# Optimization experiments

Measured on AMD Instinct MI355X. Metric: run time of the kernel, lower is better.

## Reference

```python
import jax, jax.numpy as jnp
import numpy as np

N_HEAD = 16
N_FEAT = 1024
D_K = N_FEAT // N_HEAD
BATCH = 8
SEQ = 1024
LN_EPS = 1e-5
MIN_VAL = float(np.finfo(np.float32).min)


def setup_inputs() -> dict:
    key = jax.random.key(0)
    ks = jax.random.split(key, 8)
    s = 0.02  # small init scale for weights to keep activations sane
    return {
        "x": jax.random.normal(ks[0], (BATCH, SEQ, N_FEAT), jnp.float32),
        "pos_k": jax.random.normal(ks[1], (SEQ, SEQ, D_K), jnp.float32) * s,
        "mask": jnp.ones((BATCH, SEQ, SEQ), jnp.int32),
        "ln_scale": jnp.ones((N_FEAT,), jnp.float32),
        "ln_bias": jnp.zeros((N_FEAT,), jnp.float32),
        "wq": jax.random.normal(ks[2], (N_FEAT, N_FEAT), jnp.float32) * s,
        "bq": jnp.zeros((N_FEAT,), jnp.float32),
        "wk": jax.random.normal(ks[3], (N_FEAT, N_FEAT), jnp.float32) * s,
        "bk": jnp.zeros((N_FEAT,), jnp.float32),
        "wv": jax.random.normal(ks[4], (N_FEAT, N_FEAT), jnp.float32) * s,
        "bv": jnp.zeros((N_FEAT,), jnp.float32),
        "wo": jax.random.normal(ks[5], (N_FEAT, N_FEAT), jnp.float32) * s,
        "bo": jnp.zeros((N_FEAT,), jnp.float32),
    }


def reference(x, pos_k, mask, ln_scale, ln_bias, wq, bq, wk, bk, wv, bv, wo, bo):
    b, t, f = x.shape
    h, d = N_HEAD, D_K
    # LayerNorm over feature dim
    mu = jnp.mean(x, axis=-1, keepdims=True)
    var = jnp.mean((x - mu) ** 2, axis=-1, keepdims=True)
    xn = (x - mu) / jnp.sqrt(var + LN_EPS) * ln_scale + ln_bias
    # QKV projections (torch Linear: y = x @ W^T + b), split heads -> (b, h, t, d)
    q = (xn @ wq.T + bq).reshape(b, t, h, d).transpose(0, 2, 1, 3)
    k = (xn @ wk.T + bk).reshape(b, t, h, d).transpose(0, 2, 1, 3)
    v = (xn @ wv.T + bv).reshape(b, t, h, d).transpose(0, 2, 1, 3)
    # content score A and relative-position score B
    A = jnp.einsum("bhtd,bhsd->bhts", q, k)
    B = jnp.einsum("bhtd,tsd->bhts", q, pos_k)
    scores = (A + B) / jnp.sqrt(jnp.asarray(d, scores_dtype := x.dtype))
    m = (mask[:, None, :, :] == 0)  # (b, 1, t, s) broadcast over heads
    scores = jnp.where(m, MIN_VAL, scores)
    attn = jax.nn.softmax(scores, axis=-1)
    attn = jnp.where(m, 0.0, attn)
    out = jnp.einsum("bhts,bhsd->bhtd", attn, v)
    out = out.transpose(0, 2, 1, 3).reshape(b, t, h * d)
    return out @ wo.T + bo
```

## Files before the change

kernel.cpp:

```cpp
#include <hip/hip_runtime.h>
#include <hip/hip_bf16.h>

typedef unsigned short ushort_t;
typedef short short8 __attribute__((ext_vector_type(8)));
typedef unsigned short ushort8 __attribute__((ext_vector_type(8)));
typedef unsigned short ushortx4 __attribute__((ext_vector_type(4)));
typedef float fx4 __attribute__((ext_vector_type(4)));
typedef int ix4 __attribute__((ext_vector_type(4)));

#define MFMA(a, b, c) __builtin_amdgcn_mfma_f32_16x16x32_bf16((a), (b), (c), 0, 0, 0)

#define QSCALE 0.18033688011112042f

__device__ __forceinline__ ushort_t f2bf(float f) {
  __hip_bfloat16 h = __float2bfloat16(f);
  return *(ushort_t*)&h;
}
__device__ __forceinline__ float bf2f(ushort_t h) {
  union { unsigned u; float f; } c; c.u = ((unsigned)h) << 16;
  return c.f;
}
__device__ __forceinline__ void gload16(const ushort_t* g, ushort_t* l) {
  __builtin_amdgcn_global_load_lds((const __attribute__((address_space(1))) void*)g,
                                   (__attribute__((address_space(3))) void*)l, 16, 0, 0);
}

__global__ __launch_bounds__(256) void cvt4_kernel(const float* __restrict__ s0,
                                                   const float* __restrict__ s1,
                                                   const float* __restrict__ s2,
                                                   const float* __restrict__ s3,
                                                   ushort_t* __restrict__ d0,
                                                   ushort_t* __restrict__ d1,
                                                   ushort_t* __restrict__ d2,
                                                   ushort_t* __restrict__ d3) {
  int bi = blockIdx.x;
  const float* src = (bi < 1024) ? s0 : (bi < 2048) ? s1 : (bi < 3072) ? s2 : s3;
  ushort_t* dst = (bi < 1024) ? d0 : (bi < 2048) ? d1 : (bi < 3072) ? d2 : d3;
  int i = (bi & 1023) * 256 + threadIdx.x;
  fx4 v = *(const fx4*)&src[(size_t)i * 4];
  ushortx4 o;
#pragma unroll
  for (int j = 0; j < 4; ++j) o[j] = f2bf(v[j]);
  *(ushortx4*)&dst[(size_t)i * 4] = o;
}

__global__ __launch_bounds__(256) void ln_kernel(const float* __restrict__ x,
                                                 const float* __restrict__ sc,
                                                 const float* __restrict__ bi,
                                                 ushort_t* __restrict__ xn) {
  __shared__ float red[8];
  int row = blockIdx.x, tid = threadIdx.x;
  const float* xr = x + (size_t)row * 1024;
  fx4 v = *(const fx4*)&xr[tid * 4];
  float s = v[0] + v[1] + v[2] + v[3];
  float s2 = v[0] * v[0] + v[1] * v[1] + v[2] * v[2] + v[3] * v[3];
#pragma unroll
  for (int m = 32; m >= 1; m >>= 1) {
    s += __shfl_xor(s, m);
    s2 += __shfl_xor(s2, m);
  }
  int wave = tid >> 6;
  if ((tid & 63) == 0) { red[wave * 2] = s; red[wave * 2 + 1] = s2; }
  __syncthreads();
  s = red[0] + red[2] + red[4] + red[6];
  s2 = red[1] + red[3] + red[5] + red[7];
  float mu = s * (1.f / 1024.f);
  float var = s2 * (1.f / 1024.f) - mu * mu;
  float rs = rsqrtf(var + 1e-5f);
  fx4 scv = *(const fx4*)&sc[tid * 4];
  fx4 biv = *(const fx4*)&bi[tid * 4];
  ushortx4 o;
#pragma unroll
  for (int j = 0; j < 4; ++j) o[j] = f2bf((v[j] - mu) * rs * scv[j] + biv[j]);
  *(ushortx4*)&xn[(size_t)row * 1024 + tid * 4] = o;
}

__global__ __launch_bounds__(256) void maskpack_kernel(const int* __restrict__ mask,
                                                       unsigned* __restrict__ bits) {
  __shared__ unsigned char nib[256];
  int row = blockIdx.x, tid = threadIdx.x;
  ix4 m = *(const ix4*)&mask[(size_t)row * 1024 + tid * 4];
  nib[tid] = (unsigned char)((m[0] != 0 ? 1 : 0) | (m[1] != 0 ? 2 : 0) |
                             (m[2] != 0 ? 4 : 0) | (m[3] != 0 ? 8 : 0));
  __syncthreads();
  if (tid < 32) {
    unsigned w = 0;
#pragma unroll
    for (int j = 0; j < 8; ++j) w |= ((unsigned)nib[tid * 8 + j]) << (j * 4);
    bits[(size_t)row * 32 + tid] = w;
  }
}

template <int F32OUT>
__global__ __launch_bounds__(256) void gemm_bt(const ushort_t* __restrict__ A,
                                               const ushort_t* __restrict__ B,
                                               const float* __restrict__ bias, void* C,
                                               int M, int N, int K, float oscale) {
  __shared__ ushort_t lA[4096];
  __shared__ ushort_t lB[4096];
  int bm = blockIdx.y * 128, bn = blockIdx.x * 128;
  int tid = threadIdx.x;
  int wave = tid >> 6, lane = tid & 63;
  int wm = (wave >> 1) * 64, wn = (wave & 1) * 64;
  int l15 = lane & 15, lg = lane >> 4;
  int r0 = tid >> 2, c0 = (tid & 3) * 8;
  int g1 = 256 + tid, r1 = g1 >> 2, c1 = (g1 & 3) * 8;
  int lb0 = (wave * 64) * 8;
  int lb1 = (256 + wave * 64) * 8;
  fx4 acc[4][4] = {};
  for (int k0 = 0; k0 < K; k0 += 32) {
    __syncthreads();
    gload16(&A[(size_t)(bm + r0) * K + k0 + c0], &lA[lb0]);
    gload16(&A[(size_t)(bm + r1) * K + k0 + c1], &lA[lb1]);
    gload16(&B[(size_t)(bn + r0) * K + k0 + c0], &lB[lb0]);
    gload16(&B[(size_t)(bn + r1) * K + k0 + c1], &lB[lb1]);
    __syncthreads();
    short8 af[4], bf[4];
#pragma unroll
    for (int i = 0; i < 4; ++i) af[i] = *(const short8*)&lA[(wm + i * 16 + l15) * 32 + lg * 8];
#pragma unroll
    for (int i = 0; i < 4; ++i) bf[i] = *(const short8*)&lB[(wn + i * 16 + l15) * 32 + lg * 8];
#pragma unroll
    for (int i = 0; i < 4; ++i)
#pragma unroll
      for (int j = 0; j < 4; ++j) acc[i][j] = MFMA(af[i], bf[j], acc[i][j]);
  }
#pragma unroll
  for (int j = 0; j < 4; ++j) {
    int n = bn + wn + j * 16 + l15;
    float bv = bias[n];
#pragma unroll
    for (int i = 0; i < 4; ++i) {
      int mr = bm + wm + i * 16 + lg * 4;
#pragma unroll
      for (int r = 0; r < 4; ++r) {
        float val = (acc[i][j][r] + bv) * oscale;
        if (F32OUT)
          ((float*)C)[(size_t)(mr + r) * N + n] = val;
        else
          ((ushort_t*)C)[(size_t)(mr + r) * N + n] = f2bf(val);
      }
    }
  }
}

__device__ __forceinline__ void loadset(const float* base, int c, fx4* r) {
  const float* p = base + (size_t)c * 1024;
  r[0] = *(const fx4*)p;
  r[1] = *(const fx4*)(p + 4);
  r[2] = *(const fx4*)(p + 32);
  r[3] = *(const fx4*)(p + 36);
}
__device__ __forceinline__ void cvtset(const fx4* r, short8& f0, short8& f1) {
#pragma unroll
  for (int j = 0; j < 4; ++j) {
    f0[j] = (short)f2bf(r[0][j]); f0[j + 4] = (short)f2bf(r[1][j]);
    f1[j] = (short)f2bf(r[2][j]); f1[j + 4] = (short)f2bf(r[3][j]);
  }
}

__global__ __launch_bounds__(256, 3) void ball_kernel(const ushort_t* __restrict__ q,
                                                      const float* __restrict__ pos_k,
                                                      ushort_t* __restrict__ B_all) {
  __shared__ ushort_t lq[128 * 64];
  int t = blockIdx.y, sx = blockIdx.x;
  int tid = threadIdx.x, wave = tid >> 6, lane = tid & 63, l15 = lane & 15, lg = lane >> 4;
  const float* pk = pos_k + (size_t)t * 65536;
  int sw = sx * 512 + wave * 128;
  const float* base = pk + (size_t)(sw + l15) * 64 + lg * 8;

  fx4 raw[4][4];
#pragma unroll
  for (int c = 0; c < 4; ++c) loadset(base, c, raw[c]);

#pragma unroll
  for (int it = 0; it < 4; ++it) {
    int u = tid + it * 256;
    int row = u >> 3, cu = u & 7;
    ushort8 vv = *(const ushort8*)&q[((size_t)((row >> 4) * 1024 + t)) * 1024 + (row & 15) * 64 + cu * 8];
    *(ushort8*)&lq[(row * 128 + ((cu * 16) ^ ((row & 7) << 4))) >> 1] = vv;
  }
  __syncthreads();

  short8 af0[4], af1[4];
#pragma unroll
  for (int c = 0; c < 4; ++c) cvtset(raw[c], af0[c], af1[c]);

#pragma unroll
  for (int g = 0; g < 2; ++g) {
    if (g == 0) {
#pragma unroll
      for (int c = 0; c < 4; ++c) loadset(base, 4 + c, raw[c]);
    }
    __builtin_amdgcn_sched_barrier(0);
#pragma unroll
    for (int j = 0; j < 8; ++j) {
      int row_ = j * 16 + l15;
      int cb_ = (row_ & 7) << 4;
      short8 q0 = *(const short8*)&lq[(row_ * 128 + ((lg * 16) ^ cb_)) >> 1];
      short8 q1 = *(const short8*)&lq[(row_ * 128 + ((64 + lg * 16) ^ cb_)) >> 1];
      fx4 z = {};
      size_t rb = ((size_t)row_ << 20) + (size_t)t * 1024 + (size_t)(sw + g * 64);
#pragma unroll
      for (int c = 0; c < 4; ++c) {
        fx4 a = MFMA(af0[c], q0, z);
        a = MFMA(af1[c], q1, a);
        ushortx4 o;
#pragma unroll
        for (int r = 0; r < 4; ++r) o[r] = f2bf(a[r]);
        *(ushortx4*)&B_all[rb + c * 16 + lg * 4] = o;
      }
    }
    __builtin_amdgcn_sched_barrier(0);
    if (g == 0) {
#pragma unroll
      for (int c = 0; c < 4; ++c) cvtset(raw[c], af0[c], af1[c]);
    }
  }
}

__global__ __launch_bounds__(256) void attn_kernel(const ushort_t* __restrict__ q,
                                                   const ushort_t* __restrict__ k,
                                                   const ushort_t* __restrict__ v,
                                                   const ushort_t* __restrict__ B_all,
                                                   const unsigned* __restrict__ mbits,
                                                   ushort_t* __restrict__ out) {
  __shared__ ushort_t lK[64][72];
  __shared__ ushort_t lVt[64][72];
  __shared__ ushort_t lP[4][16][72];
  int bh = blockIdx.y, b = bh >> 4, h = bh & 15;
  int t0 = blockIdx.x * 64;
  int tid = threadIdx.x, wave = tid >> 6, lane = tid & 63, l15 = lane & 15, lg = lane >> 4;
  int tw = t0 + wave * 16;
  short8 qf[2];
#pragma unroll
  for (int ks = 0; ks < 2; ++ks)
    qf[ks] = *(const short8*)&q[((size_t)(b * 1024 + tw + l15)) * 1024 + h * 64 + ks * 32 + lg * 8];
  fx4 o[4] = {};
  float lsum = 0.f;
  int trow = tw + l15;
  const unsigned* mrow = &mbits[((size_t)b * 1024 + trow) * 32];
  size_t ballrow = ((size_t)bh * 1024 + trow) * 1024;

  int rs = tid >> 3, c8g = tid & 7, c8 = c8g * 8;
  const ushort_t* kbase = &k[((size_t)(b * 1024) + rs) * 1024 + h * 64 + c8];
  const ushort_t* vbase = &v[((size_t)(b * 1024) + rs) * 1024 + h * 64 + c8];
  ushort8 kr0 = *(const ushort8*)(kbase);
  ushort8 kr1 = *(const ushort8*)(kbase + 32 * 1024);
  ushort8 vr0 = *(const ushort8*)(vbase);
  ushort8 vr1 = *(const ushort8*)(vbase + 32 * 1024);
  int vs0 = (rs + 8 * c8g) & 63;
  int vs1 = (rs + 32 + 8 * c8g) & 63;

  for (int s0 = 0; s0 < 1024; s0 += 64) {
    __syncthreads();
    *(ushort8*)&lK[rs][c8] = kr0;
    *(ushort8*)&lK[rs + 32][c8] = kr1;
#pragma unroll
    for (int j = 0; j < 8; ++j) {
      lVt[c8 + j][vs0] = vr0[j];
      lVt[c8 + j][vs1] = vr1[j];
    }
    __syncthreads();
    if (s0 + 64 < 1024) {
      size_t off = (size_t)(s0 + 64) * 1024;
      kr0 = *(const ushort8*)(kbase + off);
      kr1 = *(const ushort8*)(kbase + off + 32 * 1024);
      vr0 = *(const ushort8*)(vbase + off);
      vr1 = *(const ushort8*)(vbase + off + 32 * 1024);
    }
    __builtin_amdgcn_sched_barrier(0);
    ushortx4 b4[4];
#pragma unroll
    for (int mf = 0; mf < 4; ++mf)
      b4[mf] = *(const ushortx4*)&B_all[ballrow + s0 + mf * 16 + lg * 4];
    uint2 mw = *(const uint2*)&mrow[s0 >> 5];
    unsigned long long wb = ((unsigned long long)mw.y << 32) | mw.x;
    __builtin_amdgcn_sched_barrier(0);
    float p[16];
#pragma unroll
    for (int mf = 0; mf < 4; ++mf) {
      fx4 c4 = {};
#pragma unroll
      for (int ks = 0; ks < 2; ++ks) {
        short8 kf = *(const short8*)&lK[mf * 16 + l15][ks * 32 + lg * 8];
        c4 = MFMA(kf, qf[ks], c4);
      }
#pragma unroll
      for (int r = 0; r < 4; ++r) p[mf * 4 + r] = exp2f(c4[r] + bf2f(b4[mf][r]));
    }
    if (!__all(wb == ~0ull)) {
#pragma unroll
      for (int i = 0; i < 16; ++i) {
        int sl = (i >> 2) * 16 + lg * 4 + (i & 3);
        if (!((wb >> sl) & 1ull)) p[i] = 0.f;
      }
    }
    float ps = 0.f;
#pragma unroll
    for (int i = 0; i < 16; ++i) ps += p[i];
    lsum += ps;
#pragma unroll
    for (int mf = 0; mf < 4; ++mf) {
      ushortx4 pk4;
#pragma unroll
      for (int r = 0; r < 4; ++r) pk4[r] = f2bf(p[mf * 4 + r]);
      *(ushortx4*)&lP[wave][l15][mf * 16 + lg * 4] = pk4;
    }
#pragma unroll
    for (int ks = 0; ks < 2; ++ks) {
      short8 pf = *(const short8*)&lP[wave][l15][ks * 32 + lg * 8];
#pragma unroll
      for (int nf = 0; nf < 4; ++nf) {
        int d_ = nf * 16 + l15;
        int sb_ = (ks * 32 + lg * 8 + 8 * (d_ >> 3)) & 63;
        short8 vf = *(const short8*)&lVt[d_][sb_];
        o[nf] = MFMA(pf, vf, o[nf]);
      }
    }
  }
  lsum += __shfl_xor(lsum, 16);
  lsum += __shfl_xor(lsum, 32);
  float rl = (lsum > 0.f) ? 1.f / lsum : 0.f;
  float rw[4];
#pragma unroll
  for (int r = 0; r < 4; ++r) rw[r] = __shfl(rl, lg * 4 + r);
#pragma unroll
  for (int nf = 0; nf < 4; ++nf)
#pragma unroll
    for (int r = 0; r < 4; ++r) {
      float val = o[nf][r] * rw[r];
      out[((size_t)(b * 1024 + tw + lg * 4 + r)) * 1024 + h * 64 + nf * 16 + l15] = f2bf(val);
    }
}

extern "C" void kernel_launch(void* const* d_in, const int* in_sizes, int n_in, void* d_out,
                              int out_size, void* d_ws, size_t ws_size, hipStream_t stream) {
  (void)in_sizes; (void)n_in; (void)out_size; (void)ws_size;
  const float* x = (const float*)d_in[0];
  const float* pos_k = (const float*)d_in[1];
  const int* mask = (const int*)d_in[2];
  const float* ln_scale = (const float*)d_in[3];
  const float* ln_bias = (const float*)d_in[4];
  const float* wq = (const float*)d_in[5];
  const float* bq = (const float*)d_in[6];
  const float* wk = (const float*)d_in[7];
  const float* bk = (const float*)d_in[8];
  const float* wv = (const float*)d_in[9];
  const float* bv = (const float*)d_in[10];
  const float* wo = (const float*)d_in[11];
  const float* bo = (const float*)d_in[12];
  float* out = (float*)d_out;
  char* ws = (char*)d_ws;
  const size_t MB = 1ull << 20;
  ushort_t* xn = (ushort_t*)(ws + 0 * MB);
  ushort_t* qb = (ushort_t*)(ws + 16 * MB);
  ushort_t* kb = (ushort_t*)(ws + 32 * MB);
  ushort_t* vb = (ushort_t*)(ws + 48 * MB);
  ushort_t* ao = (ushort_t*)(ws + 64 * MB);
  ushort_t* wqb = (ushort_t*)(ws + 80 * MB);
  ushort_t* wkb = (ushort_t*)(ws + 82 * MB);
  ushort_t* wvb = (ushort_t*)(ws + 84 * MB);
  ushort_t* wob = (ushort_t*)(ws + 86 * MB);
  ushort_t* ball = (ushort_t*)(ws + 88 * MB);
  unsigned* mbits = (unsigned*)(ws + 0 * MB);

  cvt4_kernel<<<4096, 256, 0, stream>>>(wq, wk, wv, wo, wqb, wkb, wvb, wob);
  ln_kernel<<<8192, 256, 0, stream>>>(x, ln_scale, ln_bias, xn);
  dim3 gg(8, 64);
  gemm_bt<0><<<gg, 256, 0, stream>>>(xn, wqb, bq, qb, 8192, 1024, 1024, QSCALE);
  gemm_bt<0><<<gg, 256, 0, stream>>>(xn, wkb, bk, kb, 8192, 1024, 1024, 1.f);
  gemm_bt<0><<<gg, 256, 0, stream>>>(xn, wvb, bv, vb, 8192, 1024, 1024, 1.f);
  maskpack_kernel<<<8192, 256, 0, stream>>>(mask, mbits);
  ball_kernel<<<dim3(2, 1024), 256, 0, stream>>>(qb, pos_k, ball);
  attn_kernel<<<dim3(16, 128), 256, 0, stream>>>(qb, kb, vb, ball, mbits, ao);
  gemm_bt<1><<<gg, 256, 0, stream>>>(ao, wob, bo, out, 8192, 1024, 1024, 1.f);
}
```

Baseline: 430.1 us.

## Process two query tiles per wave in attention to reuse K/V tiles

Each attention block now covers 128 query rows, with every wave computing two 16-row query tiles that share the same K and V fragments loaded from LDS. This halves K/V global loads and LDS staging per query row and the grid shrinks by half. In exchange, per-thread register use roughly doubles, which may reduce occupancy, and there are fewer blocks to spread across CUs.

```diff
diff --git a/kernel.cpp b/kernel.cpp
--- a/kernel.cpp
+++ b/kernel.cpp
@@ -227,20 +227,23 @@
                                                    ushort_t* __restrict__ out) {
   __shared__ ushort_t lK[64][72];
   __shared__ ushort_t lVt[64][72];
-  __shared__ ushort_t lP[4][16][72];
+  __shared__ ushort_t lP[4][2][16][72];
   int bh = blockIdx.y, b = bh >> 4, h = bh & 15;
-  int t0 = blockIdx.x * 64;
+  int t0 = blockIdx.x * 128;
   int tid = threadIdx.x, wave = tid >> 6, lane = tid & 63, l15 = lane & 15, lg = lane >> 4;
-  int tw = t0 + wave * 16;
-  short8 qf[2];
-#pragma unroll
-  for (int ks = 0; ks < 2; ++ks)
-    qf[ks] = *(const short8*)&q[((size_t)(b * 1024 + tw + l15)) * 1024 + h * 64 + ks * 32 + lg * 8];
-  fx4 o[4] = {};
-  float lsum = 0.f;
-  int trow = tw + l15;
-  const unsigned* mrow = &mbits[((size_t)b * 1024 + trow) * 32];
-  size_t ballrow = ((size_t)bh * 1024 + trow) * 1024;
+  int twA = t0 + wave * 16, twB = twA + 64;
+  short8 qfA[2], qfB[2];
+#pragma unroll
+  for (int ks = 0; ks < 2; ++ks) {
+    qfA[ks] = *(const short8*)&q[((size_t)(b * 1024 + twA + l15)) * 1024 + h * 64 + ks * 32 + lg * 8];
+    qfB[ks] = *(const short8*)&q[((size_t)(b * 1024 + twB + l15)) * 1024 + h * 64 + ks * 32 + lg * 8];
+  }
+  fx4 oA[4] = {}, oB[4] = {};
+  float lsumA = 0.f, lsumB = 0.f;
+  const unsigned* mrowA = &mbits[((size_t)b * 1024 + twA + l15) * 32];
+  const unsigned* mrowB = &mbits[((size_t)b * 1024 + twB + l15) * 32];
+  size_t ballA = ((size_t)bh * 1024 + twA + l15) * 1024;
+  size_t ballB = ((size_t)bh * 1024 + twB + l15) * 1024;
 
   int rs = tid >> 3, c8g = tid & 7, c8 = c8g * 8;
   const ushort_t* kbase = &k[((size_t)(b * 1024) + rs) * 1024 + h * 64 + c8];
@@ -270,67 +273,88 @@
       vr1 = *(const ushort8*)(vbase + off + 32 * 1024);
     }
     __builtin_amdgcn_sched_barrier(0);
-    ushortx4 b4[4];
-#pragma unroll
-    for (int mf = 0; mf < 4; ++mf)
-      b4[mf] = *(const ushortx4*)&B_all[ballrow + s0 + mf * 16 + lg * 4];
-    uint2 mw = *(const uint2*)&mrow[s0 >> 5];
-    unsigned long long wb = ((unsigned long long)mw.y << 32) | mw.x;
+    ushortx4 b4A[4], b4B[4];
+#pragma unroll
+    for (int mf = 0; mf < 4; ++mf) {
+      b4A[mf] = *(const ushortx4*)&B_all[ballA + s0 + mf * 16 + lg * 4];
+      b4B[mf] = *(const ushortx4*)&B_all[ballB + s0 + mf * 16 + lg * 4];
+    }
+    uint2 mwA = *(const uint2*)&mrowA[s0 >> 5];
+    uint2 mwB = *(const uint2*)&mrowB[s0 >> 5];
+    unsigned long long wbA = ((unsigned long long)mwA.y << 32) | mwA.x;
+    unsigned long long wbB = ((unsigned long long)mwB.y << 32) | mwB.x;
     __builtin_amdgcn_sched_barrier(0);
-    float p[16];
+    float pA[16], pB[16];
 #pragma unroll
     for (int mf = 0; mf < 4; ++mf) {
-      fx4 c4 = {};
-#pragma unroll
-      for (int ks = 0; ks < 2; ++ks) {
-        short8 kf = *(const short8*)&lK[mf * 16 + l15][ks * 32 + lg * 8];
-        c4 = MFMA(kf, qf[ks], c4);
+      short8 kf0 = *(const short8*)&lK[mf * 16 + l15][lg * 8];
+      short8 kf1 = *(const short8*)&lK[mf * 16 + l15][32 + lg * 8];
+      fx4 cA = {}, cB = {};
+      cA = MFMA(kf0, qfA[0], cA);
+      cA = MFMA(kf1, qfA[1], cA);
+      cB = MFMA(kf0, qfB[0], cB);
+      cB = MFMA(kf1, qfB[1], cB);
+#pragma unroll
+      for (int r = 0; r < 4; ++r) {
+        pA[mf * 4 + r] = exp2f(cA[r] + bf2f(b4A[mf][r]));
+        pB[mf * 4 + r] = exp2f(cB[r] + bf2f(b4B[mf][r]));
       }
-#pragma unroll
-      for (int r = 0; r < 4; ++r) p[mf * 4 + r] = exp2f(c4[r] + bf2f(b4[mf][r]));
-    }
-    if (!__all(wb == ~0ull)) {
+    }
+    if (!__all((wbA == ~0ull) && (wbB == ~0ull))) {
 #pragma unroll
       for (int i = 0; i < 16; ++i) {
         int sl = (i >> 2) * 16 + lg * 4 + (i & 3);
-        if (!((wb >> sl) & 1ull)) p[i] = 0.f;
+        if (!((wbA >> sl) & 1ull)) pA[i] = 0.f;
+        if (!((wbB >> sl) & 1ull)) pB[i] = 0.f;
       }
     }
-    float ps = 0.f;
-#pragma unroll
-    for (int i = 0; i < 16; ++i) ps += p[i];
-    lsum += ps;
+    float psA = 0.f, psB = 0.f;
+#pragma unroll
+    for (int i = 0; i < 16; ++i) { psA += pA[i]; psB += pB[i]; }
+    lsumA += psA;
+    lsumB += psB;
 #pragma unroll
     for (int mf = 0; mf < 4; ++mf) {
-      ushortx4 pk4;
-#pragma unroll
-      for (int r = 0; r < 4; ++r) pk4[r] = f2bf(p[mf * 4 + r]);
-      *(ushortx4*)&lP[wave][l15][mf * 16 + lg * 4] = pk4;
+      ushortx4 pk4A, pk4B;
+#pragma unroll
+      for (int r = 0; r < 4; ++r) { pk4A[r] = f2bf(pA[mf * 4 + r]); pk4B[r] = f2bf(pB[mf * 4 + r]); }
+      *(ushortx4*)&lP[wave][0][l15][mf * 16 + lg * 4] = pk4A;
+      *(ushortx4*)&lP[wave][1][l15][mf * 16 + lg * 4] = pk4B;
     }
 #pragma unroll
     for (int ks = 0; ks < 2; ++ks) {
-      short8 pf = *(const short8*)&lP[wave][l15][ks * 32 + lg * 8];
+      short8 pfA = *(const short8*)&lP[wave][0][l15][ks * 32 + lg * 8];
+      short8 pfB = *(const short8*)&lP[wave][1][l15][ks * 32 + lg * 8];
 #pragma unroll
       for (int nf = 0; nf < 4; ++nf) {
         int d_ = nf * 16 + l15;
         int sb_ = (ks * 32 + lg * 8 + 8 * (d_ >> 3)) & 63;
         short8 vf = *(const short8*)&lVt[d_][sb_];
-        o[nf] = MFMA(pf, vf, o[nf]);
+        oA[nf] = MFMA(pfA, vf, oA[nf]);
+        oB[nf] = MFMA(pfB, vf, oB[nf]);
       }
     }
   }
-  lsum += __shfl_xor(lsum, 16);
-  lsum += __shfl_xor(lsum, 32);
-  float rl = (lsum > 0.f) ? 1.f / lsum : 0.f;
-  float rw[4];
-#pragma unroll
-  for (int r = 0; r < 4; ++r) rw[r] = __shfl(rl, lg * 4 + r);
+  lsumA += __shfl_xor(lsumA, 16);
+  lsumA += __shfl_xor(lsumA, 32);
+  lsumB += __shfl_xor(lsumB, 16);
+  lsumB += __shfl_xor(lsumB, 32);
+  float rlA = (lsumA > 0.f) ? 1.f / lsumA : 0.f;
+  float rlB = (lsumB > 0.f) ? 1.f / lsumB : 0.f;
+  float rwA[4], rwB[4];
+#pragma unroll
+  for (int r = 0; r < 4; ++r) {
+    rwA[r] = __shfl(rlA, lg * 4 + r);
+    rwB[r] = __shfl(rlB, lg * 4 + r);
+  }
 #pragma unroll
   for (int nf = 0; nf < 4; ++nf)
 #pragma unroll
     for (int r = 0; r < 4; ++r) {
-      float val = o[nf][r] * rw[r];
-      out[((size_t)(b * 1024 + tw + lg * 4 + r)) * 1024 + h * 64 + nf * 16 + l15] = f2bf(val);
+      out[((size_t)(b * 1024 + twA + lg * 4 + r)) * 1024 + h * 64 + nf * 16 + l15] =
+          f2bf(oA[nf][r] * rwA[r]);
+      out[((size_t)(b * 1024 + twB + lg * 4 + r)) * 1024 + h * 64 + nf * 16 + l15] =
+          f2bf(oB[nf][r] * rwB[r]);
     }
 }
 
@@ -373,6 +397,6 @@
   gemm_bt<0><<<gg, 256, 0, stream>>>(xn, wvb, bv, vb, 8192, 1024, 1024, 1.f);
   maskpack_kernel<<<8192, 256, 0, stream>>>(mask, mbits);
   ball_kernel<<<dim3(2, 1024), 256, 0, stream>>>(qb, pos_k, ball);
-  attn_kernel<<<dim3(16, 128), 256, 0, stream>>>(qb, kb, vb, ball, mbits, ao);
+  attn_kernel<<<dim3(8, 128), 256, 0, stream>>>(qb, kb, vb, ball, mbits, ao);
   gemm_bt<1><<<gg, 256, 0, stream>>>(ao, wob, bo, out, 8192, 1024, 1024, 1.f);
 }
```

Result: faster. 415.4 us (-3.4%).
